# Kernel optimization log

Hardware: AMD Instinct MI355X
Metric: run time of the kernel (lower is better)

Reference implementation:

```python
import jax, jax.numpy as jnp
import numpy as np

B, S, D, A = 16, 4096, 2048, 2048

def setup_inputs() -> dict:
    key = jax.random.key(0)
    k1, k2, k3, k4 = jax.random.split(key, 4)
    encode_state = jax.random.normal(k1, (B, S, D), dtype=jnp.float32)
    hid_state = jax.random.normal(k2, (B, D), dtype=jnp.float32)
    W = jax.random.normal(k3, (A, D), dtype=jnp.float32) * (1.0 / np.sqrt(D))
    b = jax.random.normal(k4, (A,), dtype=jnp.float32) * 0.01
    return {"encode_state": encode_state, "hid_state": hid_state, "W": W, "b": b}

def reference(encode_state, hid_state, W, b):
    # project both encoder states and decoder hidden state: y = x @ W.T + b
    enc_proj = jnp.einsum('bsd,ad->bsa', encode_state, W) + b   # [B,S,A]
    hid_proj = jnp.einsum('bd,ad->ba', hid_state, W) + b        # [B,A]
    scores = jnp.einsum('bsa,ba->bs', enc_proj, hid_proj)       # [B,S]
    probs = jax.nn.softmax(scores, axis=1)                      # softmax over seq dim
    context_vector = jnp.einsum('bs,bsd->bd', probs, encode_state)  # [B,D]
    return (scores, context_vector)
```

## Files before the change

kernel.cpp:

```cpp
#include <hip/hip_runtime.h>
#include <hip/hip_bf16.h>
#include <cstddef>
#include <cstdint>

#define BB 16
#define SS 4096
#define DD 2048
#define AA 2048
#define ACH 64
#define RPB 64
#define CHB 64

#define AS1 __attribute__((address_space(1)))
#define AS3 __attribute__((address_space(3)))

__device__ __forceinline__ void gll16(const float* g, float* l) {
  __builtin_amdgcn_global_load_lds((const AS1 uint32_t*)g, (AS3 uint32_t*)l, 16, 0, 0);
}

__device__ inline unsigned int pk_bf16(float a, float b) {
  __hip_bfloat162 h2 = __float22bfloat162_rn(make_float2(a, b));
  return *reinterpret_cast<unsigned int*>(&h2);
}

__global__ __launch_bounds__(256) void hp_kernel(
    const float* __restrict__ hid, const float* __restrict__ W,
    const float* __restrict__ bias, float* __restrict__ hp) {
  int gw   = (blockIdx.x * 256 + threadIdx.x) >> 6;
  int lane = threadIdx.x & 63;
  int a = gw;
  const float4* Wr = reinterpret_cast<const float4*>(W + (size_t)a * DD);
  float acc[BB];
#pragma unroll
  for (int b = 0; b < BB; ++b) acc[b] = 0.f;
#pragma unroll
  for (int k = 0; k < 8; ++k) {
    float4 w4 = Wr[lane + 64 * k];
#pragma unroll
    for (int b = 0; b < BB; ++b) {
      float4 h4 = reinterpret_cast<const float4*>(hid + b * DD)[lane + 64 * k];
      acc[b] += w4.x * h4.x + w4.y * h4.y + w4.z * h4.z + w4.w * h4.w;
    }
  }
  float bi = bias[a];
#pragma unroll
  for (int b = 0; b < BB; ++b) {
    float s = acc[b];
#pragma unroll
    for (int off = 32; off; off >>= 1) s += __shfl_xor(s, off, 64);
    if (lane == 0) hp[b * AA + a] = s + bi;
  }
}

__global__ __launch_bounds__(256) void vpart_kernel(
    const float* __restrict__ hp, const float* __restrict__ W,
    float* __restrict__ vpart) {
  int t  = threadIdx.x;
  int ac = blockIdx.x & 63;
  int dc = blockIdx.x >> 6;
  int d0 = dc * 1024 + 4 * t;
  float4 acc[BB];
#pragma unroll
  for (int b = 0; b < BB; ++b) acc[b] = make_float4(0.f, 0.f, 0.f, 0.f);
  int abase = ac * 32;
  for (int i = 0; i < 32; ++i) {
    int a = abase + i;
    float4 w4 = *reinterpret_cast<const float4*>(W + (size_t)a * DD + d0);
#pragma unroll
    for (int b = 0; b < BB; ++b) {
      float h = hp[b * AA + a];
      acc[b].x += h * w4.x; acc[b].y += h * w4.y;
      acc[b].z += h * w4.z; acc[b].w += h * w4.w;
    }
  }
#pragma unroll
  for (int b = 0; b < BB; ++b)
    *reinterpret_cast<float4*>(vpart + (size_t)(ac * BB + b) * DD + d0) = acc[b];
}

__global__ __launch_bounds__(256) void finalize_kernel(
    const float* __restrict__ vpart, const float* __restrict__ hp,
    const float* __restrict__ bias, float* __restrict__ v,
    float* __restrict__ cvec) {
  if (blockIdx.x < 128) {
    int i = blockIdx.x * 256 + threadIdx.x;
    float s = 0.f;
#pragma unroll
    for (int c = 0; c < ACH; ++c) s += vpart[(size_t)c * (BB * DD) + i];
    v[i] = s;
  } else {
    int b = blockIdx.x - 128;
    int t = threadIdx.x;
    float s = 0.f;
    for (int i = t; i < AA; i += 256) s += bias[i] * hp[b * AA + i];
#pragma unroll
    for (int off = 32; off; off >>= 1) s += __shfl_xor(s, off, 64);
    __shared__ float red[4];
    if ((t & 63) == 0) red[t >> 6] = s;
    __syncthreads();
    if (t == 0) cvec[b] = red[0] + red[1] + red[2] + red[3];
  }
}

__global__ void fused_kernel(
    const float* __restrict__ enc, const float* __restrict__ v,
    const float* __restrict__ cvec, float* __restrict__ scores,
    float* __restrict__ mpart, float* __restrict__ lpart,
    unsigned int* __restrict__ ctxpart ) {
  __shared__ float rowbuf[3][DD];
  __shared__ float vsh[DD];
  __shared__ float red[4];
  int tid  = threadIdx.x;
  int wv   = tid >> 6;
  int lane = tid & 63;
  int blk  = blockIdx.x;
  int b    = blk >> 6;
  int c64  = blk & 63;
  size_t row0 = (size_t)b * SS + (size_t)c64 * RPB;
  const float* rbase = enc + row0 * DD;
  int gofs = wv * 512 + lane * 4;

  gll16(v + (size_t)b * DD + gofs,        &vsh[wv * 512]);
  gll16(v + (size_t)b * DD + gofs + 256,  &vsh[wv * 512 + 256]);
  gll16(rbase + gofs,        &rowbuf[0][wv * 512]);
  gll16(rbase + gofs + 256,  &rowbuf[0][wv * 512 + 256]);
  gll16(rbase + DD + gofs,       &rowbuf[1][wv * 512]);
  gll16(rbase + DD + gofs + 256, &rowbuf[1][wv * 512 + 256]);
  asm volatile("s_waitcnt vmcnt(4)" ::: "memory");
  __builtin_amdgcn_s_barrier();
  __builtin_amdgcn_sched_barrier(0);

  const float4* vs4 = reinterpret_cast<const float4*>(vsh);
  float4 va = vs4[2 * tid];
  float4 vb = vs4[2 * tid + 1];
  float cb = cvec[b];

  float4 a0 = make_float4(0.f, 0.f, 0.f, 0.f);
  float4 a1 = make_float4(0.f, 0.f, 0.f, 0.f);
  float m_s = -1e30f, l = 0.f, myscore = 0.f;
  int slot = 0, islot = 2;

  for (int r = 0; r < RPB; ++r) {
    asm volatile("s_waitcnt vmcnt(2)" ::: "memory");
    __builtin_amdgcn_s_barrier();
    __builtin_amdgcn_sched_barrier(0);

    const float4* rp = reinterpret_cast<const float4*>(&rowbuf[slot][0]);
    float4 ra = rp[2 * tid];
    float4 rb = rp[2 * tid + 1];

    {
      int rn = (r + 2 < RPB) ? r + 2 : (RPB - 1);
      const float* g = rbase + (size_t)rn * DD + gofs;
      gll16(g,       &rowbuf[islot][wv * 512]);
      gll16(g + 256, &rowbuf[islot][wv * 512 + 256]);
    }

    float pd = ra.x * va.x + ra.y * va.y + ra.z * va.z + ra.w * va.w +
               rb.x * vb.x + rb.y * vb.y + rb.z * vb.z + rb.w * vb.w;
#pragma unroll
    for (int off = 32; off; off >>= 1) pd += __shfl_xor(pd, off, 64);
    if (lane == 0) red[wv] = pd;
    asm volatile("s_waitcnt lgkmcnt(0)" ::: "memory");
    __builtin_amdgcn_s_barrier();
    __builtin_amdgcn_sched_barrier(0);
    float score = ((red[0] + red[1]) + (red[2] + red[3])) + cb;
    if (tid == r) myscore = score;

    if (score > m_s + 40.f) {
      float rs = __expf(m_s - score);
      l *= rs;
      a0.x *= rs; a0.y *= rs; a0.z *= rs; a0.w *= rs;
      a1.x *= rs; a1.y *= rs; a1.z *= rs; a1.w *= rs;
      m_s = score;
    }
    float p = __expf(score - m_s);
    l += p;
    a0.x += p * ra.x; a0.y += p * ra.y; a0.z += p * ra.z; a0.w += p * ra.w;
    a1.x += p * rb.x; a1.y += p * rb.y; a1.z += p * rb.z; a1.w += p * rb.w;

    slot  = (slot  == 2) ? 0 : slot + 1;
    islot = (islot == 2) ? 0 : islot + 1;
  }

  asm volatile("s_waitcnt vmcnt(0)" ::: "memory");

  if (tid < RPB) scores[row0 + tid] = myscore;
  if (tid == 0) { mpart[blk] = m_s; lpart[blk] = l; }
  uint4 u;
  u.x = pk_bf16(a0.x, a0.y);
  u.y = pk_bf16(a0.z, a0.w);
  u.z = pk_bf16(a1.x, a1.y);
  u.w = pk_bf16(a1.z, a1.w);
  reinterpret_cast<uint4*>(ctxpart)[(size_t)blk * 256 + tid] = u;
}

__global__ __launch_bounds__(256) void epilogue_kernel(
    const float* __restrict__ mpart, const float* __restrict__ lpart,
    const unsigned int* __restrict__ ctxpart, float* __restrict__ ctx) {
  int b  = blockIdx.x >> 3;
  int ds = blockIdx.x & 7;
  int t  = threadIdx.x;
  __shared__ float wsm[CHB];
  int c = t & 63;
  float mt = mpart[b * CHB + c];
  float lt = lpart[b * CHB + c];
  float M = mt;
#pragma unroll
  for (int off = 32; off; off >>= 1) M = fmaxf(M, __shfl_xor(M, off, 64));
  float w  = __expf(mt - M);
  float lw = lt * w;
#pragma unroll
  for (int off = 32; off; off >>= 1) lw += __shfl_xor(lw, off, 64);
  if (t < CHB) wsm[t] = w / lw;
  __syncthreads();
  int du = ds * 128 + (t >> 1);
  bool hi = (t & 1);
  float acc = 0.f;
  const unsigned int* base = ctxpart + (size_t)b * CHB * (DD / 2) + du;
  for (int cc = 0; cc < CHB; ++cc) {
    unsigned int u = base[(size_t)cc * (DD / 2)];
    float e = __uint_as_float(hi ? (u & 0xffff0000u) : (u << 16));
    acc += wsm[cc] * e;
  }
  ctx[b * DD + ds * 256 + t] = acc;
}

extern "C" void kernel_launch(void* const* d_in, const int* in_sizes, int n_in,
                              void* d_out, int out_size, void* d_ws, size_t ws_size,
                              hipStream_t stream) {
  const float* enc  = (const float*)d_in[0];
  const float* hid  = (const float*)d_in[1];
  const float* W    = (const float*)d_in[2];
  const float* bias = (const float*)d_in[3];

  float* out_scores = (float*)d_out;
  float* out_ctx    = (float*)d_out + BB * SS;

  float* ws    = (float*)d_ws;
  float* hp    = ws;
  float* vpart = hp + BB * AA;
  float* v     = vpart + ACH * BB * DD;
  float* cvec  = v + BB * DD;
  float* mpart = cvec + BB;
  float* lpart = mpart + BB * CHB;
  unsigned int* ctxp = (unsigned int*)(lpart + BB * CHB);

  hipLaunchKernelGGL(hp_kernel,       dim3(512),  dim3(256), 0, stream, hid, W, bias, hp);
  hipLaunchKernelGGL(vpart_kernel,    dim3(128),  dim3(256), 0, stream, hp, W, vpart);
  hipLaunchKernelGGL(finalize_kernel, dim3(144),  dim3(256), 0, stream, vpart, hp, bias, v, cvec);
  hipLaunchKernelGGL(fused_kernel,    dim3(1024), dim3(256), 0, stream,
                     enc, v, cvec, out_scores, mpart, lpart, ctxp);
  hipLaunchKernelGGL(epilogue_kernel, dim3(128),  dim3(256), 0, stream,
                     mpart, lpart, ctxp, out_ctx);
}
```

Before: 170.7 us.

## Software-pipeline fused attention loop to one barrier per row

Restructures the fused score/context loop so each row's cross-wave dot-product reduction is consumed one iteration later, using a double-buffered reduction array. This cuts the per-row barriers from two to one and overlaps the reduction latency with the next row's load and dot product. It also loads the v vector straight from global memory into registers instead of staging it through LDS, and unrolls the loop by three so the ring-buffer slot indices become constants. The peeled epilogue adds code complexity, and the barrier and waitcnt ordering must be exactly right for correctness.

After: 172.1 us. Within noise of the previous version (+0.8%).

```diff
diff --git a/kernel.cpp b/kernel.cpp
--- a/kernel.cpp
+++ b/kernel.cpp
@@ -108,65 +108,87 @@
     float* __restrict__ mpart, float* __restrict__ lpart,
     unsigned int* __restrict__ ctxpart ) {
   __shared__ float rowbuf[3][DD];
-  __shared__ float vsh[DD];
-  __shared__ float red[4];
+  __shared__ float red[2][4];
   int tid  = threadIdx.x;
   int wv   = tid >> 6;
   int lane = tid & 63;
   int blk  = blockIdx.x;
   int b    = blk >> 6;
-  int c64  = blk & 63;
-  size_t row0 = (size_t)b * SS + (size_t)c64 * RPB;
+  size_t row0 = (size_t)b * SS + (size_t)(blk & 63) * RPB;
   const float* rbase = enc + row0 * DD;
   int gofs = wv * 512 + lane * 4;
 
-  gll16(v + (size_t)b * DD + gofs,        &vsh[wv * 512]);
-  gll16(v + (size_t)b * DD + gofs + 256,  &vsh[wv * 512 + 256]);
-  gll16(rbase + gofs,        &rowbuf[0][wv * 512]);
-  gll16(rbase + gofs + 256,  &rowbuf[0][wv * 512 + 256]);
-  gll16(rbase + DD + gofs,       &rowbuf[1][wv * 512]);
-  gll16(rbase + DD + gofs + 256, &rowbuf[1][wv * 512 + 256]);
-  asm volatile("s_waitcnt vmcnt(4)" ::: "memory");
-  __builtin_amdgcn_s_barrier();
-  __builtin_amdgcn_sched_barrier(0);
-
-  const float4* vs4 = reinterpret_cast<const float4*>(vsh);
-  float4 va = vs4[2 * tid];
-  float4 vb = vs4[2 * tid + 1];
+#define STAGE(rn, slot)                                                      \
+  do {                                                                       \
+    gll16(rbase + (size_t)(rn) * DD + gofs,       &rowbuf[slot][wv * 512]);  \
+    gll16(rbase + (size_t)(rn) * DD + gofs + 256, &rowbuf[slot][wv * 512 + 256]); \
+  } while (0)
+
+  float4 va = *reinterpret_cast<const float4*>(v + (size_t)b * DD + 8 * tid);
+  float4 vb = *reinterpret_cast<const float4*>(v + (size_t)b * DD + 8 * tid + 4);
   float cb = cvec[b];
+  asm volatile("s_waitcnt vmcnt(0)" ::: "memory");
+
+  STAGE(0, 0);
+  STAGE(1, 1);
 
   float4 a0 = make_float4(0.f, 0.f, 0.f, 0.f);
   float4 a1 = make_float4(0.f, 0.f, 0.f, 0.f);
+  float4 ep0 = a0, ep1 = a1;
   float m_s = -1e30f, l = 0.f, myscore = 0.f;
-  int slot = 0, islot = 2;
-
-  for (int r = 0; r < RPB; ++r) {
+
+#pragma unroll 3
+  for (int r = 0; r < RPB - 1; ++r) {
     asm volatile("s_waitcnt vmcnt(2)" ::: "memory");
-    __builtin_amdgcn_s_barrier();
-    __builtin_amdgcn_sched_barrier(0);
-
-    const float4* rp = reinterpret_cast<const float4*>(&rowbuf[slot][0]);
-    float4 ra = rp[2 * tid];
-    float4 rb = rp[2 * tid + 1];
-
-    {
-      int rn = (r + 2 < RPB) ? r + 2 : (RPB - 1);
-      const float* g = rbase + (size_t)rn * DD + gofs;
-      gll16(g,       &rowbuf[islot][wv * 512]);
-      gll16(g + 256, &rowbuf[islot][wv * 512 + 256]);
-    }
-
-    float pd = ra.x * va.x + ra.y * va.y + ra.z * va.z + ra.w * va.w +
-               rb.x * vb.x + rb.y * vb.y + rb.z * vb.z + rb.w * vb.w;
-#pragma unroll
-    for (int off = 32; off; off >>= 1) pd += __shfl_xor(pd, off, 64);
-    if (lane == 0) red[wv] = pd;
     asm volatile("s_waitcnt lgkmcnt(0)" ::: "memory");
     __builtin_amdgcn_s_barrier();
     __builtin_amdgcn_sched_barrier(0);
-    float score = ((red[0] + red[1]) + (red[2] + red[3])) + cb;
-    if (tid == r) myscore = score;
-
+    if (r + 2 < RPB) STAGE(r + 2, (r + 2) % 3);
+
+    const float4* rp = reinterpret_cast<const float4*>(&rowbuf[r % 3][0]);
+    float4 e0 = rp[2 * tid];
+    float4 e1 = rp[2 * tid + 1];
+    float pd = e0.x * va.x + e0.y * va.y + e0.z * va.z + e0.w * va.w +
+               e1.x * vb.x + e1.y * vb.y + e1.z * vb.z + e1.w * vb.w;
+#pragma unroll
+    for (int off = 32; off; off >>= 1) pd += __shfl_xor(pd, off, 64);
+    if (lane == 0) red[r & 1][wv] = pd;
+
+    if (r > 0) {
+      float score = ((red[(r - 1) & 1][0] + red[(r - 1) & 1][1]) +
+                     (red[(r - 1) & 1][2] + red[(r - 1) & 1][3])) + cb;
+      if (tid == r - 1) myscore = score;
+      if (score > m_s + 40.f) {
+        float rs = __expf(m_s - score);
+        l *= rs;
+        a0.x *= rs; a0.y *= rs; a0.z *= rs; a0.w *= rs;
+        a1.x *= rs; a1.y *= rs; a1.z *= rs; a1.w *= rs;
+        m_s = score;
+      }
+      float p = __expf(score - m_s);
+      l += p;
+      a0.x += p * ep0.x; a0.y += p * ep0.y; a0.z += p * ep0.z; a0.w += p * ep0.w;
+      a1.x += p * ep1.x; a1.y += p * ep1.y; a1.z += p * ep1.z; a1.w += p * ep1.w;
+    }
+    ep0 = e0; ep1 = e1;
+  }
+
+  asm volatile("s_waitcnt vmcnt(0)" ::: "memory");
+  asm volatile("s_waitcnt lgkmcnt(0)" ::: "memory");
+  __builtin_amdgcn_s_barrier();
+  __builtin_amdgcn_sched_barrier(0);
+  {
+    const float4* rp = reinterpret_cast<const float4*>(&rowbuf[(RPB - 1) % 3][0]);
+    float4 e0 = rp[2 * tid];
+    float4 e1 = rp[2 * tid + 1];
+    float pd = e0.x * va.x + e0.y * va.y + e0.z * va.z + e0.w * va.w +
+               e1.x * vb.x + e1.y * vb.y + e1.z * vb.z + e1.w * vb.w;
+#pragma unroll
+    for (int off = 32; off; off >>= 1) pd += __shfl_xor(pd, off, 64);
+    if (lane == 0) red[(RPB - 1) & 1][wv] = pd;
+
+    float score = ((red[0][0] + red[0][1]) + (red[0][2] + red[0][3])) + cb;
+    if (tid == RPB - 2) myscore = score;
     if (score > m_s + 40.f) {
       float rs = __expf(m_s - score);
       l *= rs;
@@ -176,14 +198,27 @@
     }
     float p = __expf(score - m_s);
     l += p;
-    a0.x += p * ra.x; a0.y += p * ra.y; a0.z += p * ra.z; a0.w += p * ra.w;
-    a1.x += p * rb.x; a1.y += p * rb.y; a1.z += p * rb.z; a1.w += p * rb.w;
-
-    slot  = (slot  == 2) ? 0 : slot + 1;
-    islot = (islot == 2) ? 0 : islot + 1;
-  }
-
-  asm volatile("s_waitcnt vmcnt(0)" ::: "memory");
+    a0.x += p * ep0.x; a0.y += p * ep0.y; a0.z += p * ep0.z; a0.w += p * ep0.w;
+    a1.x += p * ep1.x; a1.y += p * ep1.y; a1.z += p * ep1.z; a1.w += p * ep1.w;
+    ep0 = e0; ep1 = e1;
+
+    asm volatile("s_waitcnt lgkmcnt(0)" ::: "memory");
+    __builtin_amdgcn_s_barrier();
+    float score2 = ((red[1][0] + red[1][1]) + (red[1][2] + red[1][3])) + cb;
+    if (tid == RPB - 1) myscore = score2;
+    if (score2 > m_s + 40.f) {
+      float rs = __expf(m_s - score2);
+      l *= rs;
+      a0.x *= rs; a0.y *= rs; a0.z *= rs; a0.w *= rs;
+      a1.x *= rs; a1.y *= rs; a1.z *= rs; a1.w *= rs;
+      m_s = score2;
+    }
+    float p2 = __expf(score2 - m_s);
+    l += p2;
+    a0.x += p2 * ep0.x; a0.y += p2 * ep0.y; a0.z += p2 * ep0.z; a0.w += p2 * ep0.w;
+    a1.x += p2 * ep1.x; a1.y += p2 * ep1.y; a1.z += p2 * ep1.z; a1.w += p2 * ep1.w;
+  }
+#undef STAGE
 
   if (tid < RPB) scores[row0 + tid] = myscore;
   if (tid == 0) { mpart[blk] = m_s; lpart[blk] = l; }
```
